# Optimization experiments

Hardware: AMD Instinct MI355X
Metric: run time of the kernel (lower is better)

Reference implementation:

```python
import jax, jax.numpy as jnp
import numpy as np

ARITY = 4
IN_DIM = 512
OUT_DIM = 32
BATCH = 4096


def setup_inputs() -> dict:
    key = jax.random.key(0)
    k1, k2 = jax.random.split(key)
    X = jax.random.normal(k1, (BATCH, IN_DIM, ARITY), dtype=jnp.float32)
    params = jax.random.normal(k2, (IN_DIM, 2 ** ARITY, OUT_DIM), dtype=jnp.float32)
    return {"X": X, "params": params}


def reference(X, params):
    # Multilinear simplex interpolation per (batch, channel):
    # sort the arity inputs, form barycentric-style coefficients from the sorted
    # gaps, and gather the arity param rows selected by reverse-cumsum bitmasks.
    ind_sort = jnp.argsort(X, axis=2)                       # [B, G, K] ascending order
    A_sort = jnp.take_along_axis(X, ind_sort, axis=2)       # sorted values
    coef = jnp.concatenate(
        [A_sort[:, :, :1], A_sort[:, :, 1:] - A_sort[:, :, :-1]], axis=2
    )                                                        # [B, G, K]
    bits = jnp.left_shift(1, ind_sort)                       # 2**A_ind
    # reverse cumulative sum along the sorted axis -> bitmask indices into params
    idx = jnp.flip(jnp.cumsum(jnp.flip(bits, axis=2), axis=2), axis=2)  # [B, G, K]
    g = jnp.arange(params.shape[0])[None, :, None]           # channel index [1, G, 1]
    gathered = params[g, idx]                                # [B, G, K, O]
    return jnp.einsum('bgk,bgko->bgo', coef, gathered)       # [B, G, O]
```

## Files before the change

### kernel.cpp

```cpp
#include <hip/hip_runtime.h>

#define BATCH   4096
#define IN_DIM  512
#define OUT_DIM 32
#define CH      8
#define NB      64
#define NGROUP  4
#define CGRID   (IN_DIM / CH)
#define BGRID   (BATCH / (NB * NGROUP))

typedef float f32x4 __attribute__((ext_vector_type(4)));

__global__ __launch_bounds__(256) void simplex_interp_persist(
    const float* __restrict__ X,
    const float* __restrict__ params,
    float* __restrict__ out)
{
    __shared__ float lds_p[CH * 16 * OUT_DIM];
    __shared__ float lds_x[NB * CH * 4];

    const int tid = threadIdx.x;
    const int cg  = blockIdx.x & (CGRID - 1);
    const int bg  = blockIdx.x >> 6;
    const int g0  = cg * CH;
    const int b0  = bg * (NB * NGROUP);

    {
        const float* src = params + (size_t)g0 * (16 * OUT_DIM);
        #pragma unroll
        for (int k = 0; k < 4; ++k) {
            const int off = (k * 256 + tid) * 4;
            *reinterpret_cast<f32x4*>(&lds_p[off]) =
                *reinterpret_cast<const f32x4*>(src + off);
        }
    }

    const int xchunk0 = tid;
    const int xlb0    = xchunk0 >> 3;
    const int xpos0   = xchunk0 & 7;
    const int xchunk1 = 256 + tid;
    const int xlb1    = xchunk1 >> 3;
    const int xpos1   = xchunk1 & 7;

    f32x4 ra, rb;
    auto load_x = [&](int grp) {
        const size_t base = ((size_t)(b0 + grp * NB) * IN_DIM + g0) * 4;
        ra = __builtin_nontemporal_load(
            reinterpret_cast<const f32x4*>(X + base + (size_t)xlb0 * (IN_DIM * 4) + xpos0 * 4));
        rb = __builtin_nontemporal_load(
            reinterpret_cast<const f32x4*>(X + base + (size_t)xlb1 * (IN_DIM * 4) + xpos1 * 4));
    };
    auto write_x = [&]() {
        *reinterpret_cast<f32x4*>(&lds_x[xlb0 * (CH * 4) + xpos0 * 4]) = ra;
        *reinterpret_cast<f32x4*>(&lds_x[xlb1 * (CH * 4) + xpos1 * 4]) = rb;
    };

    load_x(0);
    write_x();
    __syncthreads();

    const int bq  = tid >> 6;
    const int c   = (tid >> 3) & 7;
    const int sub = tid & 7;
    const int g   = g0 + c;

    const float* ldsc = &lds_p[c * (16 * OUT_DIM) + sub * 4];
    const f32x4  p15  = *reinterpret_cast<const f32x4*>(ldsc + 15 * OUT_DIM);

    for (int grp = 0; grp < NGROUP; ++grp) {
        if (grp + 1 < NGROUP) load_x(grp + 1);

        const int bbase = b0 + grp * NB;
        #pragma unroll 4
        for (int i = 0; i < NB / 4; ++i) {
            const int lb = i * 4 + bq;
            const f32x4 xv = *reinterpret_cast<const f32x4*>(&lds_x[lb * (CH * 4) + c * 4]);

            float v0 = xv.x, v1 = xv.y, v2 = xv.z, v3 = xv.w;
            int   i0 = 0,    i1 = 1,    i2 = 2,    i3 = 3;
#define CSWAP(va, vb, ia, ib)                                            \
            {                                                            \
                bool lt = (vb) < (va);                                   \
                float tv = (va); (va) = lt ? (vb) : (va); (vb) = lt ? tv : (vb); \
                int   ti = (ia); (ia) = lt ? (ib) : (ia); (ib) = lt ? ti : (ib); \
            }
            CSWAP(v0, v1, i0, i1)
            CSWAP(v2, v3, i2, i3)
            CSWAP(v0, v2, i0, i2)
            CSWAP(v1, v3, i1, i3)
            CSWAP(v1, v2, i1, i2)
#undef CSWAP

            const float c0 = v0;
            const float c1 = v1 - v0;
            const float c2 = v2 - v1;
            const float c3 = v3 - v2;

            const int idx3 = (1 << i3);
            const int idx2 = idx3 + (1 << i2);
            const int idx1 = idx2 + (1 << i1);

            const f32x4 q1 = *reinterpret_cast<const f32x4*>(ldsc + idx1 * OUT_DIM);
            const f32x4 q2 = *reinterpret_cast<const f32x4*>(ldsc + idx2 * OUT_DIM);
            const f32x4 q3 = *reinterpret_cast<const f32x4*>(ldsc + idx3 * OUT_DIM);

            const f32x4 acc = c0 * p15 + c1 * q1 + c2 * q2 + c3 * q3;

            *reinterpret_cast<f32x4*>(
                out + ((size_t)(bbase + lb) * IN_DIM + g) * OUT_DIM + sub * 4) = acc;
        }

        __syncthreads();
        if (grp + 1 < NGROUP) write_x();
        __syncthreads();
    }
}

extern "C" void kernel_launch(void* const* d_in, const int* in_sizes, int n_in,
                              void* d_out, int out_size, void* d_ws, size_t ws_size,
                              hipStream_t stream) {
    const float* X      = (const float*)d_in[0];
    const float* params = (const float*)d_in[1];
    float*       out    = (float*)d_out;

    const int nblocks = CGRID * BGRID;
    simplex_interp_persist<<<nblocks, 256, 0, stream>>>(X, params, out);
}
```

Baseline: 54.35 us.

## Make X staging wave-private with double buffering to drop block barriers

Restructures the LDS staging of X so each wave loads and reads only its own batch rows (strided by 4), using a double-buffered per-wave LDS array. This removes the two block-wide __syncthreads per group that previously serialized all waves around the X refill. The risk is reliance on intra-wave ordering of LDS writes and reads without explicit barriers, plus doubled X LDS footprint.

```diff
diff --git a/kernel.cpp b/kernel.cpp
--- a/kernel.cpp
+++ b/kernel.cpp
@@ -11,19 +11,21 @@
 
 typedef float f32x4 __attribute__((ext_vector_type(4)));
 
-__global__ __launch_bounds__(256) void simplex_interp_persist(
+__global__ __launch_bounds__(256) void simplex_interp_wavepriv(
     const float* __restrict__ X,
     const float* __restrict__ params,
     float* __restrict__ out)
 {
     __shared__ float lds_p[CH * 16 * OUT_DIM];
-    __shared__ float lds_x[NB * CH * 4];
+    __shared__ float lds_x[2][4][16][32];
 
-    const int tid = threadIdx.x;
-    const int cg  = blockIdx.x & (CGRID - 1);
-    const int bg  = blockIdx.x >> 6;
-    const int g0  = cg * CH;
-    const int b0  = bg * (NB * NGROUP);
+    const int tid  = threadIdx.x;
+    const int w    = tid >> 6;
+    const int lane = tid & 63;
+    const int cg   = blockIdx.x & (CGRID - 1);
+    const int bg   = blockIdx.x >> 6;
+    const int g0   = cg * CH;
+    const int b0   = bg * (NB * NGROUP);
 
     {
         const float* src = params + (size_t)g0 * (16 * OUT_DIM);
@@ -35,84 +37,80 @@
         }
     }
 
-    const int xchunk0 = tid;
-    const int xlb0    = xchunk0 >> 3;
-    const int xpos0   = xchunk0 & 7;
-    const int xchunk1 = 256 + tid;
-    const int xlb1    = xchunk1 >> 3;
-    const int xpos1   = xchunk1 & 7;
+    const int i0 = lane >> 3;
+    const int p0 = lane & 7;
 
     f32x4 ra, rb;
     auto load_x = [&](int grp) {
-        const size_t base = ((size_t)(b0 + grp * NB) * IN_DIM + g0) * 4;
-        ra = __builtin_nontemporal_load(
-            reinterpret_cast<const f32x4*>(X + base + (size_t)xlb0 * (IN_DIM * 4) + xpos0 * 4));
-        rb = __builtin_nontemporal_load(
-            reinterpret_cast<const f32x4*>(X + base + (size_t)xlb1 * (IN_DIM * 4) + xpos1 * 4));
+        const int bbase = b0 + grp * NB + w;
+        const size_t o0 = ((size_t)(bbase + 4 * i0)       * IN_DIM + g0 + p0) * 4;
+        const size_t o1 = ((size_t)(bbase + 4 * (i0 + 8)) * IN_DIM + g0 + p0) * 4;
+        ra = __builtin_nontemporal_load(reinterpret_cast<const f32x4*>(X + o0));
+        rb = __builtin_nontemporal_load(reinterpret_cast<const f32x4*>(X + o1));
     };
-    auto write_x = [&]() {
-        *reinterpret_cast<f32x4*>(&lds_x[xlb0 * (CH * 4) + xpos0 * 4]) = ra;
-        *reinterpret_cast<f32x4*>(&lds_x[xlb1 * (CH * 4) + xpos1 * 4]) = rb;
+    auto write_x = [&](int buf) {
+        *reinterpret_cast<f32x4*>(&lds_x[buf][w][i0][p0 * 4])     = ra;
+        *reinterpret_cast<f32x4*>(&lds_x[buf][w][i0 + 8][p0 * 4]) = rb;
     };
 
     load_x(0);
-    write_x();
+    write_x(0);
     __syncthreads();
 
-    const int bq  = tid >> 6;
-    const int c   = (tid >> 3) & 7;
-    const int sub = tid & 7;
+    const int c   = (lane >> 3) & 7;
+    const int sub = lane & 7;
     const int g   = g0 + c;
 
     const float* ldsc = &lds_p[c * (16 * OUT_DIM) + sub * 4];
     const f32x4  p15  = *reinterpret_cast<const f32x4*>(ldsc + 15 * OUT_DIM);
 
+    int buf = 0;
     for (int grp = 0; grp < NGROUP; ++grp) {
         if (grp + 1 < NGROUP) load_x(grp + 1);
 
-        const int bbase = b0 + grp * NB;
+        const int bbase = b0 + grp * NB + w;
         #pragma unroll 4
-        for (int i = 0; i < NB / 4; ++i) {
-            const int lb = i * 4 + bq;
-            const f32x4 xv = *reinterpret_cast<const f32x4*>(&lds_x[lb * (CH * 4) + c * 4]);
+        for (int i = 0; i < 16; ++i) {
+            const f32x4 xv = *reinterpret_cast<const f32x4*>(&lds_x[buf][w][i][c * 4]);
 
             float v0 = xv.x, v1 = xv.y, v2 = xv.z, v3 = xv.w;
-            int   i0 = 0,    i1 = 1,    i2 = 2,    i3 = 3;
+            int   j0 = 0,    j1 = 1,    j2 = 2,    j3 = 3;
 #define CSWAP(va, vb, ia, ib)                                            \
             {                                                            \
                 bool lt = (vb) < (va);                                   \
                 float tv = (va); (va) = lt ? (vb) : (va); (vb) = lt ? tv : (vb); \
                 int   ti = (ia); (ia) = lt ? (ib) : (ia); (ib) = lt ? ti : (ib); \
             }
-            CSWAP(v0, v1, i0, i1)
-            CSWAP(v2, v3, i2, i3)
-            CSWAP(v0, v2, i0, i2)
-            CSWAP(v1, v3, i1, i3)
-            CSWAP(v1, v2, i1, i2)
+            CSWAP(v0, v1, j0, j1)
+            CSWAP(v2, v3, j2, j3)
+            CSWAP(v0, v2, j0, j2)
+            CSWAP(v1, v3, j1, j3)
+            CSWAP(v1, v2, j1, j2)
 #undef CSWAP
 
-            const float c0 = v0;
-            const float c1 = v1 - v0;
-            const float c2 = v2 - v1;
-            const float c3 = v3 - v2;
+            const float c0f = v0;
+            const float c1f = v1 - v0;
+            const float c2f = v2 - v1;
+            const float c3f = v3 - v2;
 
-            const int idx3 = (1 << i3);
-            const int idx2 = idx3 + (1 << i2);
-            const int idx1 = idx2 + (1 << i1);
+            const int idx3 = (1 << j3);
+            const int idx2 = idx3 + (1 << j2);
+            const int idx1 = idx2 + (1 << j1);
 
             const f32x4 q1 = *reinterpret_cast<const f32x4*>(ldsc + idx1 * OUT_DIM);
             const f32x4 q2 = *reinterpret_cast<const f32x4*>(ldsc + idx2 * OUT_DIM);
             const f32x4 q3 = *reinterpret_cast<const f32x4*>(ldsc + idx3 * OUT_DIM);
 
-            const f32x4 acc = c0 * p15 + c1 * q1 + c2 * q2 + c3 * q3;
+            const f32x4 acc = c0f * p15 + c1f * q1 + c2f * q2 + c3f * q3;
 
             *reinterpret_cast<f32x4*>(
-                out + ((size_t)(bbase + lb) * IN_DIM + g) * OUT_DIM + sub * 4) = acc;
+                out + ((size_t)(bbase + 4 * i) * IN_DIM + g) * OUT_DIM + sub * 4) = acc;
         }
 
-        __syncthreads();
-        if (grp + 1 < NGROUP) write_x();
-        __syncthreads();
+        if (grp + 1 < NGROUP) {
+            write_x(buf ^ 1);
+            buf ^= 1;
+        }
     }
 }
 
@@ -124,5 +122,5 @@
     float*       out    = (float*)d_out;
 
     const int nblocks = CGRID * BGRID;
-    simplex_interp_persist<<<nblocks, 256, 0, stream>>>(X, params, out);
+    simplex_interp_wavepriv<<<nblocks, 256, 0, stream>>>(X, params, out);
 }
```

After: 62.01 us. +14.1%, slower.
